# Performance work log

Measured on AMD Instinct MI355X. Metric: run time of the kernel, lower is better.

The kernel has to match this reference:

```python
import jax, jax.numpy as jnp
import numpy as np


def setup_inputs() -> dict:
    key = jax.random.key(0)
    ks = jax.random.split(key, 5)
    B, S, H, I, E = 4, 2048, 1024, 4096, 8
    scale_in = 1.0 / np.sqrt(H)
    scale_mid = 1.0 / np.sqrt(I)
    return {
        "x": jax.random.normal(ks[0], (B, S, H), dtype=jnp.float32),
        "w_gate": jax.random.normal(ks[1], (H, E), dtype=jnp.float32) * scale_in,
        "w1": jax.random.normal(ks[2], (E, H, I), dtype=jnp.float32) * scale_in,
        "w2": jax.random.normal(ks[3], (E, I, H), dtype=jnp.float32) * scale_mid,
        "w3": jax.random.normal(ks[4], (E, H, I), dtype=jnp.float32) * scale_in,
        "num_experts_per_tok": 2,
    }


def reference(x, w_gate, w1, w2, w3, num_experts_per_tok):
    """MoE with top-k routing and SwiGLU experts (Mixtral-style).

    x: [B, S, H]; w_gate: [H, E]; w1/w3: [E, H, I]; w2: [E, I, H].
    Returns [B, S, H]. Matches torch module output (aux_loss is a side
    attribute in the original, not returned).
    """
    B, S, H = x.shape
    E = w_gate.shape[1]
    K = num_experts_per_tok
    xf = x.reshape(-1, H)                           # [T, H]

    logits = xf @ w_gate                            # [T, E]
    probs = jax.nn.softmax(logits, axis=-1)
    topk_probs, topk_idx = jax.lax.top_k(probs, K)  # [T, K]
    topk_probs = topk_probs / topk_probs.sum(axis=-1, keepdims=True)

    # Per-token per-expert combine weight: sum over k of renormalized top-k
    # probs mapped back to expert slots. [T, E]
    comb = jnp.sum(jax.nn.one_hot(topk_idx, E, dtype=xf.dtype)
                   * topk_probs[..., None], axis=1)

    out = jnp.zeros_like(xf)
    for e in range(E):  # small fixed loop over experts
        hidden = jax.nn.silu(xf @ w1[e]) * (xf @ w3[e])  # [T, I]
        out = out + (hidden @ w2[e]) * comb[:, e:e + 1]
    return out.reshape(B, S, H)
```

## Files before the change

kernel.cpp:

```cpp
#include <hip/hip_runtime.h>

typedef unsigned short u16;
typedef __attribute__((ext_vector_type(4))) float f32x4;
typedef __attribute__((ext_vector_type(8))) short s16x8;

#define T_TOK 8192
#define HD    1024
#define ID    4096
#define NE    8
#define AK    (T_TOK * 2)
#define APAD  (AK + 256)
#define MTMAX 72

#define BAR()   __builtin_amdgcn_s_barrier()
#define SB0()   __builtin_amdgcn_sched_barrier(0)
#define PRIO1() __builtin_amdgcn_s_setprio(1)
#define PRIO0() __builtin_amdgcn_s_setprio(0)
#define WAITV6() asm volatile("s_waitcnt vmcnt(6)" ::: "memory")
#define WAITV8() asm volatile("s_waitcnt vmcnt(8)" ::: "memory")
#define LGKM0()  do { asm volatile("s_waitcnt lgkmcnt(0)" ::: "memory"); SB0(); } while (0)

__device__ __forceinline__ u16 f2bf(float f) {
  unsigned u = __builtin_bit_cast(unsigned, f);
  u += 0x7FFFu + ((u >> 16) & 1u);
  return (u16)(u >> 16);
}

__device__ __forceinline__ float bf2f(u16 v) {
  unsigned u = (unsigned)v << 16;
  return __builtin_bit_cast(float, u);
}

__device__ __forceinline__ void gld16(u16* lds, const u16* g) {
  __builtin_amdgcn_global_load_lds(
      (const __attribute__((address_space(1))) unsigned int*)g,
      (__attribute__((address_space(3))) unsigned int*)lds, 16, 0, 0);
}


__global__ void k_init(int* counts) {
  if (threadIdx.x < NE) counts[threadIdx.x] = 0;
}

__global__ void k_offsets(const int* __restrict__ counts, int* offs, int* cursors,
                          int* __restrict__ tiles, int* __restrict__ ntile) {
  if (threadIdx.x == 0) {
    int s = 0;
    for (int e = 0; e < NE; ++e) { offs[e] = s; s += counts[e]; }
    offs[NE] = s;
    int nt = 0;
    for (int e = 0; e < NE; ++e)
      for (int m0 = 0; m0 < counts[e]; m0 += 256)
        tiles[nt++] = (e << 16) | (m0 >> 8);
    ntile[0] = nt;
    for (int i = nt; i < MTMAX; ++i) tiles[i] = 0;
  }
  if (threadIdx.x < NE) cursors[threadIdx.x] = 0;
}

__global__ __launch_bounds__(256) void k_scatter(
    const int* __restrict__ tidx, const int* __restrict__ offs,
    int* cursors, int* __restrict__ list, int* __restrict__ pos) {
  int idx = blockIdx.x * 256 + threadIdx.x;
  if (idx >= AK) return;
  int e = tidx[idx];
  int p = atomicAdd(&cursors[e], 1);
  int a = offs[e] + p;
  list[a] = idx >> 1;
  pos[idx] = a;
}


__device__ __forceinline__ void tconv_block(
    const float* __restrict__ in, u16* __restrict__ out,
    int R, int C, int r0, int c0, int which, int interleave, char* smem) {
  u16 (*tile)[72] = (u16(*)[72])smem;
  int t = threadIdx.x;
  int rr = t >> 4;
  int cc4 = (t & 15) * 4;
#pragma unroll
  for (int i = 0; i < 16; ++i) {
    int r = i * 16 + rr;
    float4 v = *(const float4*)&in[(size_t)(r0 + r) * C + c0 + cc4];
    ushort4 bv;
    bv.x = f2bf(v.x); bv.y = f2bf(v.y); bv.z = f2bf(v.z); bv.w = f2bf(v.w);
    *(ushort4*)&tile[r][cc4] = bv;
  }
  __syncthreads();
  int w = t >> 6;
  int c = t & 63;
  int gc = c0 + c;
  int orow = interleave ? (((gc >> 4) << 5) + which * 16 + (gc & 15)) : gc;
  u16* obase = out + (size_t)orow * R + r0 + w * 64;
#pragma unroll
  for (int j = 0; j < 8; ++j) {
    s16x8 o;
#pragma unroll
    for (int q = 0; q < 8; ++q) o[q] = (short)tile[w * 64 + j * 8 + q][c];
    *(s16x8*)&obase[j * 8] = o;
  }
}

#define NBP_CVT 4096
#define NBP_T13 4096
#define NBP_T2  2048
#define NBP_RTR 2048

__global__ __launch_bounds__(256) void k_prep(
    const float* __restrict__ x, const float* __restrict__ wg,
    const float* __restrict__ w1, const float* __restrict__ w2,
    const float* __restrict__ w3,
    u16* __restrict__ xb, u16* __restrict__ w13b, u16* __restrict__ w2b,
    int* __restrict__ tidx, float* __restrict__ tw, int* __restrict__ counts) {
  __shared__ char smem[256 * 72 * 2];
  int bid = blockIdx.x, t = threadIdx.x;

  if (bid < NBP_CVT) {
    int idx = bid * 256 + t;
    float4 v0 = ((const float4*)x)[idx * 2];
    float4 v1 = ((const float4*)x)[idx * 2 + 1];
    s16x8 o;
    o[0] = (short)f2bf(v0.x); o[1] = (short)f2bf(v0.y);
    o[2] = (short)f2bf(v0.z); o[3] = (short)f2bf(v0.w);
    o[4] = (short)f2bf(v1.x); o[5] = (short)f2bf(v1.y);
    o[6] = (short)f2bf(v1.z); o[7] = (short)f2bf(v1.w);
    ((s16x8*)xb)[idx] = o;
    return;
  }
  if (bid < NBP_CVT + NBP_T13) {
    int r = bid - NBP_CVT;
    int bx = r & 63;
    int by = (r >> 6) & 3;
    int bz = r >> 8;
    int which = bz >> 3, e = bz & 7;
    const float* in = (which ? w3 : w1) + (size_t)e * HD * ID;
    tconv_block(in, w13b + (size_t)e * 2 * ID * HD,
                HD, ID, by * 256, bx * 64, which, 1, smem);
    return;
  }
  if (bid < NBP_CVT + NBP_T13 + NBP_T2) {
    int r = bid - NBP_CVT - NBP_T13;
    int bx = r & 15;
    int by = (r >> 4) & 15;
    int e = r >> 8;
    tconv_block(w2 + (size_t)e * ID * HD, w2b + (size_t)e * HD * ID,
                ID, HD, by * 256, bx * 64, 0, 0, smem);
    return;
  }
  {
    float* wgs = (float*)smem;
    int blockR = bid - NBP_CVT - NBP_T13 - NBP_T2;
    for (int i = t; i < NE * HD; i += 256) {
      int h = i >> 3, e = i & 7;
      wgs[e * HD + h] = wg[i];
    }
    __syncthreads();
    int lane = t & 63, wid = t >> 6;
    int tok = blockR * 4 + wid;
    const float* xr = x + (size_t)tok * HD;
    double acc[NE];
#pragma unroll
    for (int e = 0; e < NE; ++e) acc[e] = 0.0;
    for (int i = 0; i < HD / 64; ++i) {
      float xv = xr[lane + i * 64];
#pragma unroll
      for (int e = 0; e < NE; ++e)
        acc[e] += (double)xv * (double)wgs[e * HD + lane + i * 64];
    }
#pragma unroll
    for (int e = 0; e < NE; ++e)
      for (int s = 32; s >= 1; s >>= 1) acc[e] += __shfl_xor(acc[e], s, 64);
    int e0 = 0; double m0 = acc[0];
    for (int e = 1; e < NE; ++e) if (acc[e] > m0) { m0 = acc[e]; e0 = e; }
    int e1 = -1; double m1 = -1e300;
    for (int e = 0; e < NE; ++e) if (e != e0 && acc[e] > m1) { m1 = acc[e]; e1 = e; }
    if (lane == 0) {
      double d = exp(m1 - m0);
      tidx[tok * 2] = e0; tidx[tok * 2 + 1] = e1;
      tw[tok * 2] = (float)(1.0 / (1.0 + d));
      tw[tok * 2 + 1] = (float)(d / (1.0 + d));
      atomicAdd(&counts[e0], 1);
      atomicAdd(&counts[e1], 1);
    }
  }
}


#define GEMM_CORE(NTK, NITER) \
  int wr = wid >> 2, wc = wid & 3; \
  int lane15 = lane & 15, lq = lane >> 4, sw8 = lane15 & 7; \
  f32x4 acc[8][4]; \
  _Pragma("unroll") for (int m = 0; m < 8; ++m) \
    _Pragma("unroll") for (int n = 0; n < 4; ++n) acc[m][n] = (f32x4){0.f,0.f,0.f,0.f}; \
  auto stgA = [&](int bb, int h, int kt) { \
    gld16(&As[bb][(h*128 + 0*64 + wid*8) * 64], gA[h*2+0] + kt*64); \
    gld16(&As[bb][(h*128 + 1*64 + wid*8) * 64], gA[h*2+1] + kt*64); }; \
  auto stgB = [&](int bb, int h, int kt) { \
    gld16(&Bs[bb][(h*128 + 0*64 + wid*8) * 64], gB[h*2+0] + kt*64); \
    gld16(&Bs[bb][(h*128 + 1*64 + wid*8) * 64], gB[h*2+1] + kt*64); }; \
  s16x8 a[4][2], b[4][2]; \
  auto rdA = [&](int bb, int mh) { \
    _Pragma("unroll") for (int mm = 0; mm < 4; ++mm) \
      _Pragma("unroll") for (int kk = 0; kk < 2; ++kk) \
        a[mm][kk] = *(const s16x8*)&As[bb][(mh*128 + wr*64 + mm*16 + lane15)*64 + (((kk*4+lq)^sw8)*8)]; }; \
  auto rdB = [&](int bb, int fh) { \
    _Pragma("unroll") for (int ff = 0; ff < 2; ++ff) \
      _Pragma("unroll") for (int kk = 0; kk < 2; ++kk) \
        b[fh*2+ff][kk] = *(const s16x8*)&Bs[bb][(fh*128 + wc*32 + ff*16 + lane15)*64 + (((kk*4+lq)^sw8)*8)]; }; \
  auto mf = [&](int mh, int fh) { \
    _Pragma("unroll") for (int kk = 0; kk < 2; ++kk) \
      _Pragma("unroll") for (int mm = 0; mm < 4; ++mm) \
        _Pragma("unroll") for (int ff = 0; ff < 2; ++ff) \
          acc[mh*4+mm][fh*2+ff] = __builtin_amdgcn_mfma_f32_16x16x32_bf16(a[mm][kk], b[fh*2+ff][kk], acc[mh*4+mm][fh*2+ff], 0, 0, 0); }; \
   \
  stgA(0,0,0); stgB(0,0,0); stgA(0,1,0); stgB(0,1,0); stgA(1,0,1); stgB(1,0,1); \
  WAITV8(); BAR(); SB0(); \
  for (int i = 0; i < (NITER); ++i) { \
    int ku2 = (2*i+2) & ((NTK)-1), ku3 = (2*i+3) & ((NTK)-1); \
     rdA(0,0); rdB(0,0); stgA(1,1,2*i+1); WAITV6(); BAR(); LGKM0(); PRIO1(); mf(0,0); PRIO0(); BAR(); SB0(); \
     rdB(0,1); stgB(1,1,2*i+1); BAR(); LGKM0(); PRIO1(); mf(0,1); PRIO0(); BAR(); SB0(); \
     rdA(0,1); stgA(0,0,ku2); BAR(); LGKM0(); PRIO1(); mf(1,0); PRIO0(); BAR(); SB0(); \
     stgB(0,0,ku2); WAITV8(); BAR(); PRIO1(); mf(1,1); PRIO0(); BAR(); SB0(); \
     rdA(1,0); rdB(1,0); stgA(0,1,ku2); WAITV6(); BAR(); LGKM0(); PRIO1(); mf(0,0); PRIO0(); BAR(); SB0(); \
     rdB(1,1); stgB(0,1,ku2); BAR(); LGKM0(); PRIO1(); mf(0,1); PRIO0(); BAR(); SB0(); \
     rdA(1,1); stgA(1,0,ku3); BAR(); LGKM0(); PRIO1(); mf(1,0); PRIO0(); BAR(); SB0(); \
     stgB(1,0,ku3); WAITV8(); BAR(); PRIO1(); mf(1,1); PRIO0(); BAR(); SB0(); \
  }

__global__ __launch_bounds__(512, 1) void k_gemm1(
    const u16* __restrict__ xb, const u16* __restrict__ w13b,
    const int* __restrict__ list, const int* __restrict__ offs,
    const int* __restrict__ tiles, const int* __restrict__ ntile,
    u16* __restrict__ hidden) {
  int ti = blockIdx.y;
  if (ti >= ntile[0]) return;
  int packed = tiles[ti];
  int e = packed >> 16;
  int m0 = (packed & 0xFFFF) << 8;
  int aoff = offs[e];
  int cnt = offs[e + 1] - aoff;
  int n0 = blockIdx.x * 256;

  __shared__ u16 As[2][256 * 64];
  __shared__ u16 Bs[2][256 * 64];

  int tid = threadIdx.x, lane = tid & 63, wid = tid >> 6;
  int l8 = lane >> 3, c8 = lane & 7;
  int csrc = (c8 ^ l8) * 8;

  const u16* gA[4]; const u16* gB[4];
#pragma unroll
  for (int h = 0; h < 2; ++h)
#pragma unroll
    for (int c = 0; c < 2; ++c) {
      int row = h * 128 + c * 64 + wid * 8 + l8;
      int rr = m0 + row; if (rr > cnt - 1) rr = cnt - 1;
      gA[h*2+c] = xb + (size_t)list[aoff + rr] * HD + csrc;
      gB[h*2+c] = w13b + ((size_t)e * 2 * ID + n0 + row) * HD + csrc;
    }

  GEMM_CORE(HD / 64, HD / 128)

#pragma unroll
  for (int mh = 0; mh < 2; ++mh)
#pragma unroll
    for (int mm = 0; mm < 4; ++mm)
#pragma unroll
      for (int j = 0; j < 4; ++j) {
        int grow = m0 + mh * 128 + wr * 64 + mm * 16 + lq * 4 + j;
        if (grow < cnt) {
          size_t rbase = (size_t)(aoff + grow) * ID;
#pragma unroll
          for (int p = 0; p < 2; ++p) {
            float v1 = acc[mh*4+mm][2*p][j];
            float v3 = acc[mh*4+mm][2*p+1][j];
            float s = v1 / (1.0f + __expf(-v1));
            int icol = ((n0 + p * 128 + wc * 32) >> 1) + lane15;
            hidden[rbase + icol] = f2bf(s * v3);
          }
        }
      }
}

__global__ __launch_bounds__(512, 1) void k_gemm2(
    const u16* __restrict__ hidden, const u16* __restrict__ w2b,
    const int* __restrict__ offs, const int* __restrict__ tiles,
    const int* __restrict__ ntile,
    u16* __restrict__ yp0, u16* __restrict__ yp3) {
  int ti = blockIdx.y;
  if (ti >= ntile[0]) return;
  int packed = tiles[ti];
  int e = packed >> 16;
  int m0 = (packed & 0xFFFF) << 8;
  int aoff = offs[e];
  int cnt = offs[e + 1] - aoff;
  int n0 = (blockIdx.x & 3) * 256;
  int kidx = blockIdx.x >> 2;
  int kc = kidx * 1024;

  __shared__ u16 As[2][256 * 64];
  __shared__ u16 Bs[2][256 * 64];

  int tid = threadIdx.x, lane = tid & 63, wid = tid >> 6;
  int l8 = lane >> 3, c8 = lane & 7;
  int csrc = (c8 ^ l8) * 8;

  const u16* gA[4]; const u16* gB[4];
#pragma unroll
  for (int h = 0; h < 2; ++h)
#pragma unroll
    for (int c = 0; c < 2; ++c) {
      int row = h * 128 + c * 64 + wid * 8 + l8;
      gA[h*2+c] = hidden + (size_t)(aoff + m0 + row) * ID + kc + csrc;
      gB[h*2+c] = w2b + ((size_t)e * HD + n0 + row) * ID + kc + csrc;
    }

  GEMM_CORE(1024 / 64, 1024 / 128)

  u16* yp = (kidx < 3) ? yp0 + (size_t)kidx * AK * HD : yp3;
#pragma unroll
  for (int mh = 0; mh < 2; ++mh)
#pragma unroll
    for (int mm = 0; mm < 4; ++mm)
#pragma unroll
      for (int j = 0; j < 4; ++j) {
        int grow = m0 + mh * 128 + wr * 64 + mm * 16 + lq * 4 + j;
        if (grow < cnt) {
          u16* yrow = yp + (size_t)(aoff + grow) * HD;
#pragma unroll
          for (int f = 0; f < 4; ++f) {
            int col = n0 + (f >> 1) * 128 + wc * 32 + (f & 1) * 16 + lane15;
            yrow[col] = f2bf(acc[mh*4+mm][f][j]);
          }
        }
      }
}

__global__ __launch_bounds__(256) void k_combine(
    const u16* __restrict__ yp0, const u16* __restrict__ yp3,
    const int* __restrict__ pos, const float* __restrict__ tw,
    float* __restrict__ out) {
  int t = blockIdx.x;
  int c = threadIdx.x * 4;
  int a0 = pos[t * 2], a1 = pos[t * 2 + 1];
  float w0 = tw[t * 2], w1 = tw[t * 2 + 1];
  float s0[4] = {0.f, 0.f, 0.f, 0.f}, s1[4] = {0.f, 0.f, 0.f, 0.f};
#pragma unroll
  for (int k = 0; k < 4; ++k) {
    const u16* yp = (k < 3) ? yp0 + (size_t)k * AK * HD : yp3;
    ushort4 v0 = *(const ushort4*)&yp[(size_t)a0 * HD + c];
    ushort4 v1 = *(const ushort4*)&yp[(size_t)a1 * HD + c];
    s0[0] += bf2f(v0.x); s0[1] += bf2f(v0.y); s0[2] += bf2f(v0.z); s0[3] += bf2f(v0.w);
    s1[0] += bf2f(v1.x); s1[1] += bf2f(v1.y); s1[2] += bf2f(v1.z); s1[3] += bf2f(v1.w);
  }
  float4 o;
  o.x = w0 * s0[0] + w1 * s1[0];
  o.y = w0 * s0[1] + w1 * s1[1];
  o.z = w0 * s0[2] + w1 * s1[2];
  o.w = w0 * s0[3] + w1 * s1[3];
  *(float4*)&out[(size_t)t * HD + c] = o;
}


extern "C" void kernel_launch(void* const* d_in, const int* in_sizes, int n_in,
                              void* d_out, int out_size, void* d_ws, size_t ws_size,
                              hipStream_t stream) {
  const float* x  = (const float*)d_in[0];
  const float* wg = (const float*)d_in[1];
  const float* w1 = (const float*)d_in[2];
  const float* w2 = (const float*)d_in[3];
  const float* w3 = (const float*)d_in[4];

  char* p = (char*)d_ws;
  auto alloc = [&](size_t bytes) {
    char* r = p;
    p += (bytes + 255) & ~(size_t)255;
    return r;
  };
  u16*   xb      = (u16*)alloc((size_t)T_TOK * HD * 2);
  u16*   w13b    = (u16*)alloc((size_t)NE * 2 * ID * HD * 2);
  u16*   w2b     = (u16*)alloc((size_t)NE * HD * ID * 2);
  u16*   hidden  = (u16*)alloc((size_t)APAD * ID * 2);
  u16*   yp3     = (u16*)alloc((size_t)AK * HD * 2);
  int*   tidx    = (int*)alloc(AK * 4);
  float* tw      = (float*)alloc(AK * 4);
  int*   list    = (int*)alloc(AK * 4);
  int*   pos     = (int*)alloc(AK * 4);
  int*   counts  = (int*)alloc(64);
  int*   offs    = (int*)alloc(64);
  int*   cursors = (int*)alloc(64);
  int*   tiles   = (int*)alloc(MTMAX * 4);
  int*   ntile   = (int*)alloc(64);
  (void)ws_size; (void)in_sizes; (void)n_in; (void)out_size;

  u16* yp0 = w13b;

  k_init<<<1, 64, 0, stream>>>(counts);
  k_prep<<<NBP_CVT + NBP_T13 + NBP_T2 + NBP_RTR, 256, 0, stream>>>(
      x, wg, w1, w2, w3, xb, w13b, w2b, tidx, tw, counts);
  k_offsets<<<1, 64, 0, stream>>>(counts, offs, cursors, tiles, ntile);
  k_scatter<<<AK / 256, 256, 0, stream>>>(tidx, offs, cursors, list, pos);

  dim3 gg1(2 * ID / 256, MTMAX, 1);
  k_gemm1<<<gg1, 512, 0, stream>>>(xb, w13b, list, offs, tiles, ntile, hidden);
  dim3 gg2(16, MTMAX, 1);
  k_gemm2<<<gg2, 512, 0, stream>>>(hidden, w2b, offs, tiles, ntile, yp0, yp3);
  k_combine<<<T_TOK, 256, 0, stream>>>(yp0, yp3, pos, tw, (float*)d_out);
}
```

Measured before the change: 888.9 us.

## Fuse x bf16 conversion into router, move w2 transpose into gemm1, stage epilogues in LDS

The x-to-bf16 conversion now happens inside the router blocks, which already read x, so the separate conversion blocks and their extra pass over x are gone. The w2 transpose/convert moves out of k_prep into extra blocks of the k_gemm1 grid, so that weight preparation can overlap with the first grouped GEMM. Both GEMM epilogues now stage results through LDS and write 16-byte row-contiguous vectors instead of scattered 2-byte stores. The trade-offs are extra barriers and LDS traffic in the epilogue, and w2 conversion blocks that compete with GEMM blocks for CUs.

```diff
diff --git a/kernel.cpp b/kernel.cpp
--- a/kernel.cpp
+++ b/kernel.cpp
@@ -71,85 +71,51 @@
 }
 
 
-__device__ __forceinline__ void tconv_block(
-    const float* __restrict__ in, u16* __restrict__ out,
-    int R, int C, int r0, int c0, int which, int interleave, char* smem) {
-  u16 (*tile)[72] = (u16(*)[72])smem;
-  int t = threadIdx.x;
-  int rr = t >> 4;
-  int cc4 = (t & 15) * 4;
-#pragma unroll
-  for (int i = 0; i < 16; ++i) {
-    int r = i * 16 + rr;
-    float4 v = *(const float4*)&in[(size_t)(r0 + r) * C + c0 + cc4];
-    ushort4 bv;
-    bv.x = f2bf(v.x); bv.y = f2bf(v.y); bv.z = f2bf(v.z); bv.w = f2bf(v.w);
-    *(ushort4*)&tile[r][cc4] = bv;
-  }
-  __syncthreads();
-  int w = t >> 6;
-  int c = t & 63;
-  int gc = c0 + c;
-  int orow = interleave ? (((gc >> 4) << 5) + which * 16 + (gc & 15)) : gc;
-  u16* obase = out + (size_t)orow * R + r0 + w * 64;
-#pragma unroll
-  for (int j = 0; j < 8; ++j) {
-    s16x8 o;
-#pragma unroll
-    for (int q = 0; q < 8; ++q) o[q] = (short)tile[w * 64 + j * 8 + q][c];
-    *(s16x8*)&obase[j * 8] = o;
-  }
-}
-
-#define NBP_CVT 4096
 #define NBP_T13 4096
-#define NBP_T2  2048
 #define NBP_RTR 2048
 
 __global__ __launch_bounds__(256) void k_prep(
     const float* __restrict__ x, const float* __restrict__ wg,
-    const float* __restrict__ w1, const float* __restrict__ w2,
-    const float* __restrict__ w3,
-    u16* __restrict__ xb, u16* __restrict__ w13b, u16* __restrict__ w2b,
+    const float* __restrict__ w1, const float* __restrict__ w3,
+    u16* __restrict__ xb, u16* __restrict__ w13b,
     int* __restrict__ tidx, float* __restrict__ tw, int* __restrict__ counts) {
   __shared__ char smem[256 * 72 * 2];
   int bid = blockIdx.x, t = threadIdx.x;
 
-  if (bid < NBP_CVT) {
-    int idx = bid * 256 + t;
-    float4 v0 = ((const float4*)x)[idx * 2];
-    float4 v1 = ((const float4*)x)[idx * 2 + 1];
-    s16x8 o;
-    o[0] = (short)f2bf(v0.x); o[1] = (short)f2bf(v0.y);
-    o[2] = (short)f2bf(v0.z); o[3] = (short)f2bf(v0.w);
-    o[4] = (short)f2bf(v1.x); o[5] = (short)f2bf(v1.y);
-    o[6] = (short)f2bf(v1.z); o[7] = (short)f2bf(v1.w);
-    ((s16x8*)xb)[idx] = o;
-    return;
-  }
-  if (bid < NBP_CVT + NBP_T13) {
-    int r = bid - NBP_CVT;
-    int bx = r & 63;
-    int by = (r >> 6) & 3;
-    int bz = r >> 8;
+  if (bid < NBP_T13) {
+    u16 (*tile)[72] = (u16(*)[72])smem;
+    int bx = bid & 63;
+    int by = (bid >> 6) & 3;
+    int bz = bid >> 8;
     int which = bz >> 3, e = bz & 7;
     const float* in = (which ? w3 : w1) + (size_t)e * HD * ID;
-    tconv_block(in, w13b + (size_t)e * 2 * ID * HD,
-                HD, ID, by * 256, bx * 64, which, 1, smem);
-    return;
-  }
-  if (bid < NBP_CVT + NBP_T13 + NBP_T2) {
-    int r = bid - NBP_CVT - NBP_T13;
-    int bx = r & 15;
-    int by = (r >> 4) & 15;
-    int e = r >> 8;
-    tconv_block(w2 + (size_t)e * ID * HD, w2b + (size_t)e * HD * ID,
-                ID, HD, by * 256, bx * 64, 0, 0, smem);
+    int r0 = by * 256, c0 = bx * 64;
+    int rr = t >> 4, cc4 = (t & 15) * 4;
+#pragma unroll
+    for (int i = 0; i < 16; ++i) {
+      int r = i * 16 + rr;
+      float4 v = *(const float4*)&in[(size_t)(r0 + r) * ID + c0 + cc4];
+      ushort4 bv;
+      bv.x = f2bf(v.x); bv.y = f2bf(v.y); bv.z = f2bf(v.z); bv.w = f2bf(v.w);
+      *(ushort4*)&tile[r][cc4] = bv;
+    }
+    __syncthreads();
+    int w = t >> 6, c = t & 63;
+    int gc = c0 + c;
+    int orow = ((gc >> 4) << 5) + which * 16 + (gc & 15);
+    u16* obase = w13b + ((size_t)e * 2 * ID + orow) * HD + r0 + w * 64;
+#pragma unroll
+    for (int j = 0; j < 8; ++j) {
+      s16x8 o;
+#pragma unroll
+      for (int q = 0; q < 8; ++q) o[q] = (short)tile[w * 64 + j * 8 + q][c];
+      *(s16x8*)&obase[j * 8] = o;
+    }
     return;
   }
   {
     float* wgs = (float*)smem;
-    int blockR = bid - NBP_CVT - NBP_T13 - NBP_T2;
+    int blockR = bid - NBP_T13;
     for (int i = t; i < NE * HD; i += 256) {
       int h = i >> 3, e = i & 7;
       wgs[e * HD + h] = wg[i];
@@ -158,11 +124,13 @@
     int lane = t & 63, wid = t >> 6;
     int tok = blockR * 4 + wid;
     const float* xr = x + (size_t)tok * HD;
+    u16* xo = xb + (size_t)tok * HD;
     double acc[NE];
 #pragma unroll
     for (int e = 0; e < NE; ++e) acc[e] = 0.0;
     for (int i = 0; i < HD / 64; ++i) {
       float xv = xr[lane + i * 64];
+      xo[lane + i * 64] = f2bf(xv);
 #pragma unroll
       for (int e = 0; e < NE; ++e)
         acc[e] += (double)xv * (double)wgs[e * HD + lane + i * 64];
@@ -227,11 +195,46 @@
      stgB(1,0,ku3); WAITV8(); BAR(); PRIO1(); mf(1,1); PRIO0(); BAR(); SB0(); \
   }
 
+
 __global__ __launch_bounds__(512, 1) void k_gemm1(
     const u16* __restrict__ xb, const u16* __restrict__ w13b,
     const int* __restrict__ list, const int* __restrict__ offs,
     const int* __restrict__ tiles, const int* __restrict__ ntile,
-    u16* __restrict__ hidden) {
+    u16* __restrict__ hidden,
+    const float* __restrict__ w2, u16* __restrict__ w2b) {
+  __shared__ u16 As[2][256 * 64];
+  __shared__ u16 Bs[2][256 * 64];
+  int tid = threadIdx.x, lane = tid & 63, wid = tid >> 6;
+
+  if (blockIdx.y >= MTMAX) {
+    u16 (*tile)[64] = (u16(*)[64])&As[0][0];
+    int flat = (blockIdx.y - MTMAX) * 32 + blockIdx.x;
+    int bx = flat & 15, by = (flat >> 4) & 15, e2 = flat >> 8;
+    const float* in = w2 + (size_t)e2 * ID * HD;
+    u16* outp = w2b + (size_t)e2 * HD * ID;
+    int r0 = by * 256, c0 = bx * 64;
+    int rr = tid >> 4, cc4 = (tid & 15) * 4;
+#pragma unroll
+    for (int i = 0; i < 8; ++i) {
+      int r = i * 32 + rr;
+      float4 v = *(const float4*)&in[(size_t)(r0 + r) * HD + c0 + cc4];
+      ushort4 bv;
+      bv.x = f2bf(v.x); bv.y = f2bf(v.y); bv.z = f2bf(v.z); bv.w = f2bf(v.w);
+      *(ushort4*)&tile[r][cc4] = bv;
+    }
+    __syncthreads();
+    int w = tid >> 6, c = tid & 63;
+    u16* obase = outp + (size_t)(c0 + c) * ID + r0 + w * 32;
+#pragma unroll
+    for (int j = 0; j < 4; ++j) {
+      s16x8 o;
+#pragma unroll
+      for (int q = 0; q < 8; ++q) o[q] = (short)tile[w * 32 + j * 8 + q][c];
+      *(s16x8*)&obase[j * 8] = o;
+    }
+    return;
+  }
+
   int ti = blockIdx.y;
   if (ti >= ntile[0]) return;
   int packed = tiles[ti];
@@ -241,10 +244,6 @@
   int cnt = offs[e + 1] - aoff;
   int n0 = blockIdx.x * 256;
 
-  __shared__ u16 As[2][256 * 64];
-  __shared__ u16 Bs[2][256 * 64];
-
-  int tid = threadIdx.x, lane = tid & 63, wid = tid >> 6;
   int l8 = lane >> 3, c8 = lane & 7;
   int csrc = (c8 ^ l8) * 8;
 
@@ -261,25 +260,34 @@
 
   GEMM_CORE(HD / 64, HD / 128)
 
+  u16 (*Ls)[132] = (u16(*)[132])&As[0][0];
+  BAR();
 #pragma unroll
   for (int mh = 0; mh < 2; ++mh)
 #pragma unroll
     for (int mm = 0; mm < 4; ++mm)
 #pragma unroll
       for (int j = 0; j < 4; ++j) {
-        int grow = m0 + mh * 128 + wr * 64 + mm * 16 + lq * 4 + j;
-        if (grow < cnt) {
-          size_t rbase = (size_t)(aoff + grow) * ID;
-#pragma unroll
-          for (int p = 0; p < 2; ++p) {
-            float v1 = acc[mh*4+mm][2*p][j];
-            float v3 = acc[mh*4+mm][2*p+1][j];
-            float s = v1 / (1.0f + __expf(-v1));
-            int icol = ((n0 + p * 128 + wc * 32) >> 1) + lane15;
-            hidden[rbase + icol] = f2bf(s * v3);
-          }
+        int rl = mh * 128 + wr * 64 + mm * 16 + lq * 4 + j;
+#pragma unroll
+        for (int p = 0; p < 2; ++p) {
+          float v1 = acc[mh*4+mm][2*p][j];
+          float v3 = acc[mh*4+mm][2*p+1][j];
+          float s = v1 / (1.0f + __expf(-v1));
+          Ls[rl][p * 64 + wc * 16 + lane15] = f2bf(s * v3);
         }
       }
+  BAR();
+#pragma unroll
+  for (int ps = 0; ps < 8; ++ps) {
+    int r = ps * 32 + (tid >> 4);
+    int grow = m0 + r;
+    if (grow < cnt) {
+      int cl = (tid & 15) * 8;
+      *(s16x8*)&hidden[(size_t)(aoff + grow) * ID + (n0 >> 1) + cl] =
+          *(const s16x8*)&Ls[r][cl];
+    }
+  }
 }
 
 __global__ __launch_bounds__(512, 1) void k_gemm2(
@@ -318,22 +326,35 @@
   GEMM_CORE(1024 / 64, 1024 / 128)
 
   u16* yp = (kidx < 3) ? yp0 + (size_t)kidx * AK * HD : yp3;
-#pragma unroll
-  for (int mh = 0; mh < 2; ++mh)
-#pragma unroll
-    for (int mm = 0; mm < 4; ++mm)
-#pragma unroll
-      for (int j = 0; j < 4; ++j) {
-        int grow = m0 + mh * 128 + wr * 64 + mm * 16 + lq * 4 + j;
-        if (grow < cnt) {
-          u16* yrow = yp + (size_t)(aoff + grow) * HD;
-#pragma unroll
-          for (int f = 0; f < 4; ++f) {
-            int col = n0 + (f >> 1) * 128 + wc * 32 + (f & 1) * 16 + lane15;
-            yrow[col] = f2bf(acc[mh*4+mm][f][j]);
+  u16 (*Ls)[132] = (u16(*)[132])&As[0][0];
+#pragma unroll
+  for (int half = 0; half < 2; ++half) {
+    BAR();
+#pragma unroll
+    for (int mh = 0; mh < 2; ++mh)
+#pragma unroll
+      for (int mm = 0; mm < 4; ++mm)
+#pragma unroll
+        for (int j = 0; j < 4; ++j) {
+          int rl = mh * 128 + wr * 64 + mm * 16 + lq * 4 + j;
+#pragma unroll
+          for (int fo = 0; fo < 2; ++fo) {
+            int f = half * 2 + fo;
+            Ls[rl][wc * 32 + fo * 16 + lane15] = f2bf(acc[mh*4+mm][f][j]);
           }
         }
+    BAR();
+#pragma unroll
+    for (int ps = 0; ps < 8; ++ps) {
+      int r = ps * 32 + (tid >> 4);
+      int grow = m0 + r;
+      if (grow < cnt) {
+        int cl = (tid & 15) * 8;
+        *(s16x8*)&yp[(size_t)(aoff + grow) * HD + n0 + half * 128 + cl] =
+            *(const s16x8*)&Ls[r][cl];
       }
+    }
+  }
 }
 
 __global__ __launch_bounds__(256) void k_combine(
@@ -396,13 +417,14 @@
   u16* yp0 = w13b;
 
   k_init<<<1, 64, 0, stream>>>(counts);
-  k_prep<<<NBP_CVT + NBP_T13 + NBP_T2 + NBP_RTR, 256, 0, stream>>>(
-      x, wg, w1, w2, w3, xb, w13b, w2b, tidx, tw, counts);
+  k_prep<<<NBP_T13 + NBP_RTR, 256, 0, stream>>>(
+      x, wg, w1, w3, xb, w13b, tidx, tw, counts);
   k_offsets<<<1, 64, 0, stream>>>(counts, offs, cursors, tiles, ntile);
   k_scatter<<<AK / 256, 256, 0, stream>>>(tidx, offs, cursors, list, pos);
 
-  dim3 gg1(2 * ID / 256, MTMAX, 1);
-  k_gemm1<<<gg1, 512, 0, stream>>>(xb, w13b, list, offs, tiles, ntile, hidden);
+  dim3 gg1(2 * ID / 256, MTMAX + 64, 1);
+  k_gemm1<<<gg1, 512, 0, stream>>>(xb, w13b, list, offs, tiles, ntile, hidden,
+                                   w2, w2b);
   dim3 gg2(16, MTMAX, 1);
   k_gemm2<<<gg2, 512, 0, stream>>>(hidden, w2b, offs, tiles, ntile, yp0, yp3);
   k_combine<<<T_TOK, 256, 0, stream>>>(yp0, yp3, pos, tw, (float*)d_out);
```

Result: faster. 870.0 us (-2.1%).
